# Performance work log

Measured on AMD Instinct MI355X. Metric: run time of the kernel, lower is better.

The kernel has to match this reference:

```python
import jax, jax.numpy as jnp
import numpy as np

B, S, NI, H = 64, 200, 50000, 256

def setup_inputs() -> dict:
    key = jax.random.key(0)
    ks = jax.random.split(key, 10)
    # trailing-padded sequences: lengths in [S//2, S]
    lengths = jax.random.randint(ks[0], (B,), S // 2, S + 1)
    t = jnp.arange(S)
    valid = t[None, :] < lengths[:, None]
    items = jnp.where(valid, jax.random.randint(ks[1], (B, S), 1, NI), 0)
    actions = jnp.where(valid, jax.random.randint(ks[2], (B, S), 0, 2), 0)
    sc = 1.0 / np.sqrt(H)
    # W_ih of nn.LSTM is [4H, 2*NI]; store transposed [2*NI, 4H] so one-hot matmul == row gather
    WihT = jax.random.uniform(ks[3], (2 * NI, 4 * H), jnp.float32, -sc, sc)
    Whh = jax.random.uniform(ks[4], (4 * H, H), jnp.float32, -sc, sc)
    b_lstm = jax.random.uniform(ks[5], (4 * H,), jnp.float32, -sc, sc)  # b_ih + b_hh
    trans_emb = jax.random.normal(ks[6], (NI, H), jnp.float32) * 0.05
    trans_emb = trans_emb.at[0].set(0.0)  # padding_idx=0
    Wq = jax.random.normal(ks[7], (2, H), jnp.float32) * sc
    bq = jnp.zeros((2,), jnp.float32)
    return {"items": items, "actions": actions, "WihT": WihT, "Whh": Whh,
            "b_lstm": b_lstm, "trans_emb": trans_emb, "Wq": Wq, "bq": bq}

def reference(items, actions, WihT, Whh, b_lstm, trans_emb, Wq, bq):
    ni = trans_emb.shape[0]
    h_dim = Whh.shape[1]
    it = items[:, :-1]    # [B,T]
    ac = actions[:, :-1]  # [B,T]
    mask = (it != 0)      # [B,T]
    # cat(one_hot(items,NI), one_hot(actions,NI)) @ W_ih.T == gather of two rows of WihT
    x_proj = (WihT[it] + WihT[ni + ac]) * mask[..., None].astype(WihT.dtype)  # [B,T,4H]

    def step(carry, inp):
        h, c = carry
        xp, m = inp  # xp: [B,4H], m: [B] bool
        gates = xp + h @ Whh.T + b_lstm
        i, f, g, o = jnp.split(gates, 4, axis=-1)  # torch gate order: i,f,g,o
        i = jax.nn.sigmoid(i); f = jax.nn.sigmoid(f)
        g = jnp.tanh(g);       o = jax.nn.sigmoid(o)
        c_new = f * c + i * g
        h_new = o * jnp.tanh(c_new)
        m = m[:, None]
        c = jnp.where(m, c_new, c)   # packed seq: state frozen past length
        h = jnp.where(m, h_new, h)
        out = jnp.where(m, h_new, 0.0)  # pad_packed pads outputs with zeros
        return (h, c), out

    b = items.shape[0]
    h0 = jnp.zeros((b, h_dim), WihT.dtype)
    (_, _), outs = jax.lax.scan(step, (h0, h0), (jnp.swapaxes(x_proj, 0, 1), mask.T))
    states = jnp.swapaxes(outs, 0, 1)  # [B,T,H]

    q_it = items[:, 1:]
    emb = trans_emb.at[0].set(0.0)[q_it]          # padding_idx=0 -> zero row
    query = (emb * states) @ Wq.T + bq            # [B,T,2]
    valid = (q_it != 0)
    targets = jnp.where(valid, actions[:, 1:], 0)
    logp = jax.nn.log_softmax(query, axis=-1)
    nll = -jnp.take_along_axis(logp, targets[..., None], axis=-1)[..., 0]
    vf = valid.astype(nll.dtype)
    # masked mean == F.cross_entropy over gathered (rows, cols) logits
    loss = jnp.sum(nll * vf) / jnp.sum(vf)
    return loss
```

## Files before the change

kernel.cpp:

```cpp
#include <hip/hip_runtime.h>
#include <stdint.h>

#define NITEMS 50000
#define SEQ    200
#define TMAX   199


template<int CTRL>
__device__ __forceinline__ float dpp_add(float x) {
    int r = __builtin_amdgcn_update_dpp(0, __float_as_int(x), CTRL, 0xF, 0xF, true);
    return x + __int_as_float(r);
}

__global__ __launch_bounds__(512, 2)
void lstm_main(const int* __restrict__ items, const int* __restrict__ actions,
               const float* __restrict__ WihT, const float* __restrict__ Whh,
               const float* __restrict__ b_lstm, const float* __restrict__ trans_emb,
               const float* __restrict__ Wq, const float* __restrict__ bq,
               int* flags, float* h_buf, float* accum)
{
    const int bid  = blockIdx.x;
    const int g    = (bid & 7) + 8 * ((bid >> 3) >> 2);
    const int q    = (bid >> 3) & 3;
    const int tid  = threadIdx.x;
    const int lane = tid & 63;
    const int wv   = tid >> 6;
    const int rg   = tid >> 4;
    const int kc   = tid & 15;

    __shared__ float xp_lds[2][256];
    __shared__ float gate_lds[256];
    __shared__ float b_lds[256];
    __shared__ float emb_lds[2][256];
    __shared__ float wq_lds[2][256];
    __shared__ float bq_lds[2];
    __shared__ int   items_s[SEQ];
    __shared__ int   act_s[SEQ];
    __shared__ int   len_sh;

    for (int i = tid; i < SEQ; i += 512) {
        items_s[i] = items[g * SEQ + i];
        act_s[i]   = actions[g * SEQ + i];
    }
    if (tid < 256) {
        b_lds[tid] = b_lstm[(tid >> 6) * 256 + q * 64 + (tid & 63)];
    } else {
        const int k = tid - 256;
        wq_lds[0][k] = Wq[k];
        wq_lds[1][k] = Wq[256 + k];
    }
    if (tid == 0) { bq_lds[0] = bq[0]; bq_lds[1] = bq[1]; }
    __syncthreads();
    if (tid == 0) {
        int L = 0;
        while (L < SEQ && items_s[L] != 0) ++L;
        len_sh = L;
    }
    __syncthreads();
    const int len = len_sh;
    const int L   = min(len, TMAX);

    float wgt[8][16];
    #pragma unroll
    for (int r = 0; r < 8; ++r) {
        const int r_blk = rg * 8 + r;
        const int j = (r_blk >> 6) * 256 + q * 64 + (r_blk & 63);
        const float4* wp = (const float4*)(Whh + (size_t)j * 256 + kc * 16);
        #pragma unroll
        for (int m = 0; m < 4; ++m) {
            float4 v = wp[m];
            wgt[r][4*m+0] = v.x; wgt[r][4*m+1] = v.y;
            wgt[r][4*m+2] = v.z; wgt[r][4*m+3] = v.w;
        }
    }

    if (wv == 0) {
        const int it = items_s[0], ac = act_s[0];
        const int c = lane >> 4, off = (lane & 15) * 4;
        float4 va = *(const float4*)(WihT + (size_t)it * 1024 + c * 256 + q * 64 + off);
        float4 vb = *(const float4*)(WihT + (size_t)(NITEMS + ac) * 1024 + c * 256 + q * 64 + off);
        *(float4*)&xp_lds[0][c * 64 + off] =
            make_float4(va.x+vb.x, va.y+vb.y, va.z+vb.z, va.w+vb.w);
    }
    if (q == 0 && wv == 2) {
        const int qe = items_s[1];
        float4 e = make_float4(0.f,0.f,0.f,0.f);
        if (qe != 0) e = *(const float4*)(trans_emb + (size_t)qe * 256 + 4 * lane);
        *(float4*)&emb_lds[0][4 * lane] = e;
    }
    __syncthreads();

    float c_cell = 0.f;
    float nll_acc = 0.f, cnt_acc = 0.f;
    float hreg[16];
    #pragma unroll
    for (int m = 0; m < 16; ++m) hreg[m] = 0.f;

    int*   myflags = flags + g * 32;
    float* hb      = h_buf + (size_t)g * 512;

    for (int t = 0; t < L; ++t) {
        if (t > 0) {
            if (tid < 4 && tid != q) {
                int guard = 0;
                while (__hip_atomic_load(&myflags[tid], __ATOMIC_ACQUIRE,
                                         __HIP_MEMORY_SCOPE_AGENT) < t) {
                    __builtin_amdgcn_s_sleep(1);
                    if (++guard > (1 << 16)) break;
                }
            }
            __syncthreads();
            unsigned long long* hp = (unsigned long long*)(hb + (t & 1) * 256 + kc * 16);
            #pragma unroll
            for (int m = 0; m < 8; ++m) {
                unsigned long long u = __hip_atomic_load(&hp[m], __ATOMIC_RELAXED,
                                                         __HIP_MEMORY_SCOPE_AGENT);
                union { unsigned long long u; float f[2]; } cv; cv.u = u;
                hreg[2*m]   = cv.f[0];
                hreg[2*m+1] = cv.f[1];
            }
        }

        const int tn = t + 1;
        float4 xa = make_float4(0,0,0,0), xb = make_float4(0,0,0,0);
        float4 ev = make_float4(0,0,0,0);
        float  he[4] = {0,0,0,0};
        if (wv == 1 && tn < L) {
            const int it = items_s[tn], ac = act_s[tn];
            const int c = lane >> 4, off = (lane & 15) * 4;
            xa = *(const float4*)(WihT + (size_t)it * 1024 + c * 256 + q * 64 + off);
            xb = *(const float4*)(WihT + (size_t)(NITEMS + ac) * 1024 + c * 256 + q * 64 + off);
        }
        if (q == 0 && wv == 2) {
            const int qe = items_s[tn];
            if (qe != 0) ev = *(const float4*)(trans_emb + (size_t)qe * 256 + 4 * lane);
            if (t >= 1) {
                unsigned long long* hp2 = (unsigned long long*)(hb + (t & 1) * 256 + 4 * lane);
                unsigned long long u0 = __hip_atomic_load(&hp2[0], __ATOMIC_RELAXED,
                                                          __HIP_MEMORY_SCOPE_AGENT);
                unsigned long long u1 = __hip_atomic_load(&hp2[1], __ATOMIC_RELAXED,
                                                          __HIP_MEMORY_SCOPE_AGENT);
                union { unsigned long long u; float f[2]; } c0, c1; c0.u = u0; c1.u = u1;
                he[0] = c0.f[0]; he[1] = c0.f[1]; he[2] = c1.f[0]; he[3] = c1.f[1];
            }
        }

        float acc[8];
        #pragma unroll
        for (int r = 0; r < 8; ++r) acc[r] = 0.f;
        #pragma unroll
        for (int m = 0; m < 16; ++m) {
            #pragma unroll
            for (int r = 0; r < 8; ++r) acc[r] = fmaf(wgt[r][m], hreg[m], acc[r]);
        }
        #pragma unroll
        for (int r = 0; r < 8; ++r) {
            float v = acc[r];
            v = dpp_add<0x128>(v);
            v = dpp_add<0x124>(v);
            v = dpp_add<0x122>(v);
            v = dpp_add<0x121>(v);
            acc[r] = v;
        }
        if (kc == 0) {
            #pragma unroll
            for (int r = 0; r < 8; ++r) {
                const int r_blk = rg * 8 + r;
                gate_lds[r_blk] = acc[r] + xp_lds[t & 1][r_blk] + b_lds[r_blk];
            }
        }
        __syncthreads();

        if (tid < 64) {
            const int d = tid;
            float gi = gate_lds[d];
            float gf = gate_lds[64 + d];
            float gg = gate_lds[128 + d];
            float go = gate_lds[192 + d];
            float ii = 1.f / (1.f + __expf(-gi));
            float ff = 1.f / (1.f + __expf(-gf));
            float oo = 1.f / (1.f + __expf(-go));
            float gt = tanhf(gg);
            c_cell = ff * c_cell + ii * gt;
            float hn = oo * tanhf(c_cell);
            __hip_atomic_store(&hb[((t + 1) & 1) * 256 + q * 64 + d], hn,
                               __ATOMIC_RELAXED, __HIP_MEMORY_SCOPE_AGENT);
            if (d == 0)
                __hip_atomic_store(&myflags[q], t + 1,
                                   __ATOMIC_RELEASE, __HIP_MEMORY_SCOPE_AGENT);
        } else if (wv == 1) {
            if (tn < L) {
                const int c = lane >> 4, off = (lane & 15) * 4;
                *(float4*)&xp_lds[tn & 1][c * 64 + off] =
                    make_float4(xa.x+xb.x, xa.y+xb.y, xa.z+xb.z, xa.w+xb.w);
            }
        } else if (wv == 2 && q == 0) {
            if (t >= 1) {
                const float* eb = &emb_lds[(t - 1) & 1][0];
                float s0 = 0.f, s1 = 0.f;
                #pragma unroll
                for (int m = 0; m < 4; ++m) {
                    const int k = 4 * lane + m;
                    float p = eb[k] * he[m];
                    s0 = fmaf(p, wq_lds[0][k], s0);
                    s1 = fmaf(p, wq_lds[1][k], s1);
                }
                #pragma unroll
                for (int off2 = 32; off2; off2 >>= 1) {
                    s0 += __shfl_xor(s0, off2);
                    s1 += __shfl_xor(s1, off2);
                }
                if (lane == 0) {
                    const int tgt = act_s[t];
                    float z0 = s0 + bq_lds[0], z1 = s1 + bq_lds[1];
                    float mz = fmaxf(z0, z1);
                    float lse = mz + __logf(__expf(z0 - mz) + __expf(z1 - mz));
                    nll_acc += lse - (tgt ? z1 : z0);
                    cnt_acc += 1.f;
                }
            }
            *(float4*)&emb_lds[t & 1][4 * lane] = ev;
        }
        __syncthreads();
    }

    if (q == 0 && wv == 2) {
        if (items_s[L] != 0) {
            if (lane < 4) {
                int guard = 0;
                while (__hip_atomic_load(&myflags[lane], __ATOMIC_ACQUIRE,
                                         __HIP_MEMORY_SCOPE_AGENT) < L) {
                    __builtin_amdgcn_s_sleep(1);
                    if (++guard > (1 << 16)) break;
                }
            }
            unsigned long long* hp2 = (unsigned long long*)(hb + (L & 1) * 256 + 4 * lane);
            unsigned long long u0 = __hip_atomic_load(&hp2[0], __ATOMIC_RELAXED,
                                                      __HIP_MEMORY_SCOPE_AGENT);
            unsigned long long u1 = __hip_atomic_load(&hp2[1], __ATOMIC_RELAXED,
                                                      __HIP_MEMORY_SCOPE_AGENT);
            union { unsigned long long u; float f[2]; } c0, c1; c0.u = u0; c1.u = u1;
            float he2[4] = { c0.f[0], c0.f[1], c1.f[0], c1.f[1] };
            const float* eb = &emb_lds[(L - 1) & 1][0];
            float s0 = 0.f, s1 = 0.f;
            #pragma unroll
            for (int m = 0; m < 4; ++m) {
                const int k = 4 * lane + m;
                float p = eb[k] * he2[m];
                s0 = fmaf(p, wq_lds[0][k], s0);
                s1 = fmaf(p, wq_lds[1][k], s1);
            }
            #pragma unroll
            for (int off2 = 32; off2; off2 >>= 1) {
                s0 += __shfl_xor(s0, off2);
                s1 += __shfl_xor(s1, off2);
            }
            if (lane == 0) {
                const int tgt = act_s[L];
                float z0 = s0 + bq_lds[0], z1 = s1 + bq_lds[1];
                float mz = fmaxf(z0, z1);
                float lse = mz + __logf(__expf(z0 - mz) + __expf(z1 - mz));
                nll_acc += lse - (tgt ? z1 : z0);
                cnt_acc += 1.f;
            }
        }
        if (lane == 0) {
            atomicAdd(&accum[0], nll_acc);
            atomicAdd(&accum[1], cnt_acc);
        }
    }
}

__global__ void finalize_k(const float* __restrict__ accum, float* __restrict__ out) {
    out[0] = accum[0] / accum[1];
}

extern "C" void kernel_launch(void* const* d_in, const int* in_sizes, int n_in,
                              void* d_out, int out_size, void* d_ws, size_t ws_size,
                              hipStream_t stream)
{
    const int*   items     = (const int*)d_in[0];
    const int*   actions   = (const int*)d_in[1];
    const float* WihT      = (const float*)d_in[2];
    const float* Whh       = (const float*)d_in[3];
    const float* b_lstm    = (const float*)d_in[4];
    const float* trans_emb = (const float*)d_in[5];
    const float* Wq        = (const float*)d_in[6];
    const float* bq        = (const float*)d_in[7];

    char*  ws    = (char*)d_ws;
    int*   flags = (int*)ws;
    float* accum = (float*)(ws + 8192);
    float* h_buf = (float*)(ws + 12288);

    hipMemsetAsync(d_ws, 0, 12288 + 64 * 2 * 256 * 4, stream);

    lstm_main<<<dim3(256), dim3(512), 0, stream>>>(
        items, actions, WihT, Whh, b_lstm, trans_emb, Wq, bq, flags, h_buf, accum);
    finalize_k<<<dim3(1), dim3(1), 0, stream>>>(accum, (float*)d_out);
}
```

Measured before the change: 1.499 ms.

## Batch four sequences per workgroup with packed FMA and wave-wide flag polling

New measurement: 3.568 ms. +137.9%, slower.

```diff
diff --git a/kernel.cpp b/kernel.cpp
--- a/kernel.cpp
+++ b/kernel.cpp
@@ -4,12 +4,22 @@
 #define NITEMS 50000
 #define SEQ    200
 #define TMAX   199
+#define NB     4
+
+typedef float v2f __attribute__((ext_vector_type(2)));
+typedef unsigned long long u64;
 
 
 template<int CTRL>
 __device__ __forceinline__ float dpp_add(float x) {
     int r = __builtin_amdgcn_update_dpp(0, __float_as_int(x), CTRL, 0xF, 0xF, true);
     return x + __int_as_float(r);
+}
+
+__device__ __forceinline__ void ld_h2(const u64* p, float* d) {
+    u64 a = __hip_atomic_load(p, __ATOMIC_RELAXED, __HIP_MEMORY_SCOPE_AGENT);
+    union { u64 u; float f[2]; } c; c.u = a;
+    d[0] = c.f[0]; d[1] = c.f[1];
 }
 
 __global__ __launch_bounds__(512, 2)
@@ -20,27 +30,29 @@
                int* flags, float* h_buf, float* accum)
 {
     const int bid  = blockIdx.x;
-    const int g    = (bid & 7) + 8 * ((bid >> 3) >> 2);
     const int q    = (bid >> 3) & 3;
+    const int g    = (bid & 7) + 8 * (bid >> 5);
+    const int g4   = g * 4;
     const int tid  = threadIdx.x;
     const int lane = tid & 63;
     const int wv   = tid >> 6;
     const int rg   = tid >> 4;
     const int kc   = tid & 15;
 
-    __shared__ float xp_lds[2][256];
-    __shared__ float gate_lds[256];
+    __shared__ float xp_lds[2][NB][256];
+    __shared__ float gate_lds[NB][256];
     __shared__ float b_lds[256];
-    __shared__ float emb_lds[2][256];
+    __shared__ float emb_lds[2][NB][256];
     __shared__ float wq_lds[2][256];
-    __shared__ float bq_lds[2];
-    __shared__ int   items_s[SEQ];
-    __shared__ int   act_s[SEQ];
-    __shared__ int   len_sh;
-
-    for (int i = tid; i < SEQ; i += 512) {
-        items_s[i] = items[g * SEQ + i];
-        act_s[i]   = actions[g * SEQ + i];
+    __shared__ float bq_s[2];
+    __shared__ int   items_s[NB][SEQ];
+    __shared__ int   act_s[NB][SEQ];
+    __shared__ int   L_lds[NB];
+
+    for (int i = tid; i < NB * SEQ; i += 512) {
+        const int jj = i / SEQ, pos = i - jj * SEQ;
+        items_s[jj][pos] = items[(g4 + jj) * SEQ + pos];
+        act_s[jj][pos]   = actions[(g4 + jj) * SEQ + pos];
     }
     if (tid < 256) {
         b_lds[tid] = b_lstm[(tid >> 6) * 256 + q * 64 + (tid & 63)];
@@ -49,18 +61,19 @@
         wq_lds[0][k] = Wq[k];
         wq_lds[1][k] = Wq[256 + k];
     }
-    if (tid == 0) { bq_lds[0] = bq[0]; bq_lds[1] = bq[1]; }
+    if (tid == 0) { bq_s[0] = bq[0]; bq_s[1] = bq[1]; }
     __syncthreads();
-    if (tid == 0) {
-        int L = 0;
-        while (L < SEQ && items_s[L] != 0) ++L;
-        len_sh = L;
+    if (tid < NB) {
+        int Lj = 0;
+        while (Lj < SEQ && items_s[tid][Lj] != 0) ++Lj;
+        L_lds[tid] = min(Lj, TMAX);
     }
     __syncthreads();
-    const int len = len_sh;
-    const int L   = min(len, TMAX);
-
-    float wgt[8][16];
+    int Lr[NB]; int Lmax = 0;
+    #pragma unroll
+    for (int jj = 0; jj < NB; ++jj) { Lr[jj] = L_lds[jj]; Lmax = max(Lmax, Lr[jj]); }
+
+    v2f wgt2[8][8];
     #pragma unroll
     for (int r = 0; r < 8; ++r) {
         const int r_blk = rg * 8 + r;
@@ -69,139 +82,223 @@
         #pragma unroll
         for (int m = 0; m < 4; ++m) {
             float4 v = wp[m];
-            wgt[r][4*m+0] = v.x; wgt[r][4*m+1] = v.y;
-            wgt[r][4*m+2] = v.z; wgt[r][4*m+3] = v.w;
-        }
-    }
-
-    if (wv == 0) {
-        const int it = items_s[0], ac = act_s[0];
+            wgt2[r][2*m]   = (v2f){v.x, v.y};
+            wgt2[r][2*m+1] = (v2f){v.z, v.w};
+        }
+    }
+
+    if (wv >= 1 && wv <= 4) {
+        const int jj = wv - 1;
+        const int it = items_s[jj][0], ac = act_s[jj][0];
         const int c = lane >> 4, off = (lane & 15) * 4;
         float4 va = *(const float4*)(WihT + (size_t)it * 1024 + c * 256 + q * 64 + off);
         float4 vb = *(const float4*)(WihT + (size_t)(NITEMS + ac) * 1024 + c * 256 + q * 64 + off);
-        *(float4*)&xp_lds[0][c * 64 + off] =
+        *(float4*)&xp_lds[0][jj][c * 64 + off] =
             make_float4(va.x+vb.x, va.y+vb.y, va.z+vb.z, va.w+vb.w);
     }
-    if (q == 0 && wv == 2) {
-        const int qe = items_s[1];
-        float4 e = make_float4(0.f,0.f,0.f,0.f);
-        if (qe != 0) e = *(const float4*)(trans_emb + (size_t)qe * 256 + 4 * lane);
-        *(float4*)&emb_lds[0][4 * lane] = e;
-    }
     __syncthreads();
 
-    float c_cell = 0.f;
+    float c_cell[NB];
+    #pragma unroll
+    for (int jj = 0; jj < NB; ++jj) c_cell[jj] = 0.f;
     float nll_acc = 0.f, cnt_acc = 0.f;
-    float hreg[16];
+    v2f hr2[NB][8];
     #pragma unroll
-    for (int m = 0; m < 16; ++m) hreg[m] = 0.f;
-
-    int*   myflags = flags + g * 32;
-    float* hb      = h_buf + (size_t)g * 512;
-
-    for (int t = 0; t < L; ++t) {
+    for (int jj = 0; jj < NB; ++jj)
+        #pragma unroll
+        for (int m = 0; m < 8; ++m) hr2[jj][m] = (v2f){0.f, 0.f};
+
+    for (int t = 0; t < Lmax; ++t) {
         if (t > 0) {
-            if (tid < 4 && tid != q) {
-                int guard = 0;
-                while (__hip_atomic_load(&myflags[tid], __ATOMIC_ACQUIRE,
-                                         __HIP_MEMORY_SCOPE_AGENT) < t) {
-                    __builtin_amdgcn_s_sleep(1);
-                    if (++guard > (1 << 16)) break;
-                }
-            }
-            __syncthreads();
-            unsigned long long* hp = (unsigned long long*)(hb + (t & 1) * 256 + kc * 16);
-            #pragma unroll
-            for (int m = 0; m < 8; ++m) {
-                unsigned long long u = __hip_atomic_load(&hp[m], __ATOMIC_RELAXED,
-                                                         __HIP_MEMORY_SCOPE_AGENT);
-                union { unsigned long long u; float f[2]; } cv; cv.u = u;
-                hreg[2*m]   = cv.f[0];
-                hreg[2*m+1] = cv.f[1];
+            const int jjp = (lane >> 2) & 3, pp = lane & 3;
+            const bool need = (lane < 16) && (pp != q) && (t < L_lds[jjp]);
+            const int* fp = &flags[(g4 + jjp) * 32 + pp];
+            int guard = 0;
+            for (;;) {
+                int v = need ? __hip_atomic_load(fp, __ATOMIC_RELAXED,
+                                                 __HIP_MEMORY_SCOPE_AGENT)
+                             : 0x7fffffff;
+                if (__all(v >= t)) break;
+                __builtin_amdgcn_s_sleep(1);
+                if (++guard > (1 << 17)) break;
+            }
+            __threadfence();
+
+            #pragma unroll
+            for (int jj = 0; jj < NB; ++jj) {
+                if (t < Lr[jj]) {
+                    const u64* hp = (const u64*)(h_buf + (size_t)(g4 + jj) * 512
+                                                 + (t & 1) * 256 + kc * 16);
+                    #pragma unroll
+                    for (int m = 0; m < 8; ++m) {
+                        float d2[2];
+                        ld_h2(hp + m, d2);
+                        hr2[jj][m] = (v2f){d2[0], d2[1]};
+                    }
+                }
             }
         }
 
         const int tn = t + 1;
-        float4 xa = make_float4(0,0,0,0), xb = make_float4(0,0,0,0);
-        float4 ev = make_float4(0,0,0,0);
-        float  he[4] = {0,0,0,0};
-        if (wv == 1 && tn < L) {
-            const int it = items_s[tn], ac = act_s[tn];
-            const int c = lane >> 4, off = (lane & 15) * 4;
-            xa = *(const float4*)(WihT + (size_t)it * 1024 + c * 256 + q * 64 + off);
-            xb = *(const float4*)(WihT + (size_t)(NITEMS + ac) * 1024 + c * 256 + q * 64 + off);
-        }
-        if (q == 0 && wv == 2) {
-            const int qe = items_s[tn];
-            if (qe != 0) ev = *(const float4*)(trans_emb + (size_t)qe * 256 + 4 * lane);
-            if (t >= 1) {
-                unsigned long long* hp2 = (unsigned long long*)(hb + (t & 1) * 256 + 4 * lane);
-                unsigned long long u0 = __hip_atomic_load(&hp2[0], __ATOMIC_RELAXED,
-                                                          __HIP_MEMORY_SCOPE_AGENT);
-                unsigned long long u1 = __hip_atomic_load(&hp2[1], __ATOMIC_RELAXED,
-                                                          __HIP_MEMORY_SCOPE_AGENT);
-                union { unsigned long long u; float f[2]; } c0, c1; c0.u = u0; c1.u = u1;
-                he[0] = c0.f[0]; he[1] = c0.f[1]; he[2] = c1.f[0]; he[3] = c1.f[1];
-            }
-        }
-
-        float acc[8];
+        float4 xa, xb;
+        float4 ev[NB];
+        float  her[2][4];
+        if (wv >= 1 && wv <= 4) {
+            const int jj = wv - 1;
+            if (tn < L_lds[jj]) {
+                const int it = items_s[jj][tn], ac = act_s[jj][tn];
+                const int c = lane >> 4, off = (lane & 15) * 4;
+                xa = *(const float4*)(WihT + (size_t)it * 1024 + c * 256 + q * 64 + off);
+                xb = *(const float4*)(WihT + (size_t)(NITEMS + ac) * 1024 + c * 256 + q * 64 + off);
+            }
+        } else if (wv == 5 && q == 0) {
+            #pragma unroll
+            for (int jj = 0; jj < NB; ++jj) {
+                if (t < Lr[jj]) {
+                    const int qe = items_s[jj][t + 1];
+                    ev[jj] = make_float4(0.f, 0.f, 0.f, 0.f);
+                    if (qe != 0)
+                        ev[jj] = *(const float4*)(trans_emb + (size_t)qe * 256 + 4 * lane);
+                }
+            }
+        } else if ((wv == 6 || wv == 7) && q == 0 && t > 0) {
+            #pragma unroll
+            for (int jb = 0; jb < 2; ++jb) {
+                const int jj = ((wv - 6) << 1) + jb;
+                if (t < L_lds[jj]) {
+                    const u64* hp = (const u64*)(h_buf + (size_t)(g4 + jj) * 512
+                                                 + (t & 1) * 256 + 4 * lane);
+                    ld_h2(hp,     &her[jb][0]);
+                    ld_h2(hp + 1, &her[jb][2]);
+                }
+            }
+        }
+
         #pragma unroll
-        for (int r = 0; r < 8; ++r) acc[r] = 0.f;
+        for (int jj = 0; jj < NB; ++jj) {
+            if (t < Lr[jj]) {
+                v2f acc2[8];
+                #pragma unroll
+                for (int r = 0; r < 8; ++r) acc2[r] = (v2f){0.f, 0.f};
+                #pragma unroll
+                for (int m = 0; m < 8; ++m)
+                    #pragma unroll
+                    for (int r = 0; r < 8; ++r)
+                        acc2[r] = __builtin_elementwise_fma(wgt2[r][m], hr2[jj][m], acc2[r]);
+                #pragma unroll
+                for (int r = 0; r < 8; ++r) {
+                    float v = acc2[r].x + acc2[r].y;
+                    v = dpp_add<0x128>(v);
+                    v = dpp_add<0x124>(v);
+                    v = dpp_add<0x122>(v);
+                    v = dpp_add<0x121>(v);
+                    if (kc == 0) {
+                        const int r_blk = rg * 8 + r;
+                        gate_lds[jj][r_blk] = v + xp_lds[t & 1][jj][r_blk] + b_lds[r_blk];
+                    }
+                }
+            }
+        }
+        __syncthreads();
+
+        if (tid < 64) {
+            const int d = lane;
+            #pragma unroll
+            for (int jj = 0; jj < NB; ++jj) {
+                if (t < Lr[jj]) {
+                    float gi = gate_lds[jj][d];
+                    float gf = gate_lds[jj][64 + d];
+                    float gg = gate_lds[jj][128 + d];
+                    float go = gate_lds[jj][192 + d];
+                    float ii = 1.f / (1.f + __expf(-gi));
+                    float ff = 1.f / (1.f + __expf(-gf));
+                    float oo = 1.f / (1.f + __expf(-go));
+                    float gt = tanhf(gg);
+                    c_cell[jj] = ff * c_cell[jj] + ii * gt;
+                    float hn = oo * tanhf(c_cell[jj]);
+                    __hip_atomic_store(&h_buf[(size_t)(g4 + jj) * 512
+                                              + ((t + 1) & 1) * 256 + q * 64 + d],
+                                       hn, __ATOMIC_RELAXED, __HIP_MEMORY_SCOPE_AGENT);
+                }
+            }
+            if (lane < NB) {
+                if (t < L_lds[lane])
+                    __hip_atomic_store(&flags[(g4 + lane) * 32 + q], t + 1,
+                                       __ATOMIC_RELEASE, __HIP_MEMORY_SCOPE_AGENT);
+            }
+        } else if (wv >= 1 && wv <= 4) {
+            const int jj = wv - 1;
+            if (tn < L_lds[jj]) {
+                const int c = lane >> 4, off = (lane & 15) * 4;
+                *(float4*)&xp_lds[tn & 1][jj][c * 64 + off] =
+                    make_float4(xa.x+xb.x, xa.y+xb.y, xa.z+xb.z, xa.w+xb.w);
+            }
+        } else if (wv == 5 && q == 0) {
+            #pragma unroll
+            for (int jj = 0; jj < NB; ++jj) {
+                if (t < Lr[jj])
+                    *(float4*)&emb_lds[t & 1][jj][4 * lane] = ev[jj];
+            }
+        } else if ((wv == 6 || wv == 7) && q == 0 && t > 0) {
+            #pragma unroll
+            for (int jb = 0; jb < 2; ++jb) {
+                const int jj = ((wv - 6) << 1) + jb;
+                if (t < L_lds[jj]) {
+                    const float* eb = &emb_lds[(t - 1) & 1][jj][0];
+                    float s0 = 0.f, s1 = 0.f;
+                    #pragma unroll
+                    for (int m = 0; m < 4; ++m) {
+                        const int k = 4 * lane + m;
+                        float p = eb[k] * her[jb][m];
+                        s0 = fmaf(p, wq_lds[0][k], s0);
+                        s1 = fmaf(p, wq_lds[1][k], s1);
+                    }
+                    #pragma unroll
+                    for (int off2 = 32; off2; off2 >>= 1) {
+                        s0 += __shfl_xor(s0, off2);
+                        s1 += __shfl_xor(s1, off2);
+                    }
+                    if (lane == 0) {
+                        const int tgt = act_s[jj][t];
+                        float z0 = s0 + bq_s[0], z1 = s1 + bq_s[1];
+                        float mz = fmaxf(z0, z1);
+                        float lse = mz + __logf(__expf(z0 - mz) + __expf(z1 - mz));
+                        nll_acc += lse - (tgt ? z1 : z0);
+                        cnt_acc += 1.f;
+                    }
+                }
+            }
+        }
+        __syncthreads();
+    }
+
+    if (q == 0 && (wv == 6 || wv == 7)) {
         #pragma unroll
-        for (int m = 0; m < 16; ++m) {
-            #pragma unroll
-            for (int r = 0; r < 8; ++r) acc[r] = fmaf(wgt[r][m], hreg[m], acc[r]);
-        }
-        #pragma unroll
-        for (int r = 0; r < 8; ++r) {
-            float v = acc[r];
-            v = dpp_add<0x128>(v);
-            v = dpp_add<0x124>(v);
-            v = dpp_add<0x122>(v);
-            v = dpp_add<0x121>(v);
-            acc[r] = v;
-        }
-        if (kc == 0) {
-            #pragma unroll
-            for (int r = 0; r < 8; ++r) {
-                const int r_blk = rg * 8 + r;
-                gate_lds[r_blk] = acc[r] + xp_lds[t & 1][r_blk] + b_lds[r_blk];
-            }
-        }
-        __syncthreads();
-
-        if (tid < 64) {
-            const int d = tid;
-            float gi = gate_lds[d];
-            float gf = gate_lds[64 + d];
-            float gg = gate_lds[128 + d];
-            float go = gate_lds[192 + d];
-            float ii = 1.f / (1.f + __expf(-gi));
-            float ff = 1.f / (1.f + __expf(-gf));
-            float oo = 1.f / (1.f + __expf(-go));
-            float gt = tanhf(gg);
-            c_cell = ff * c_cell + ii * gt;
-            float hn = oo * tanhf(c_cell);
-            __hip_atomic_store(&hb[((t + 1) & 1) * 256 + q * 64 + d], hn,
-                               __ATOMIC_RELAXED, __HIP_MEMORY_SCOPE_AGENT);
-            if (d == 0)
-                __hip_atomic_store(&myflags[q], t + 1,
-                                   __ATOMIC_RELEASE, __HIP_MEMORY_SCOPE_AGENT);
-        } else if (wv == 1) {
-            if (tn < L) {
-                const int c = lane >> 4, off = (lane & 15) * 4;
-                *(float4*)&xp_lds[tn & 1][c * 64 + off] =
-                    make_float4(xa.x+xb.x, xa.y+xb.y, xa.z+xb.z, xa.w+xb.w);
-            }
-        } else if (wv == 2 && q == 0) {
-            if (t >= 1) {
-                const float* eb = &emb_lds[(t - 1) & 1][0];
+        for (int jb = 0; jb < 2; ++jb) {
+            const int jj = ((wv - 6) << 1) + jb;
+            const int Lj = L_lds[jj];
+            if (items_s[jj][Lj] != 0) {
+                if (lane < 4) {
+                    int guard = 0;
+                    while (__hip_atomic_load(&flags[(g4 + jj) * 32 + lane],
+                                             __ATOMIC_RELAXED,
+                                             __HIP_MEMORY_SCOPE_AGENT) < Lj) {
+                        __builtin_amdgcn_s_sleep(1);
+                        if (++guard > (1 << 17)) break;
+                    }
+                }
+                __threadfence();
+                const u64* hp = (const u64*)(h_buf + (size_t)(g4 + jj) * 512
+                                             + (Lj & 1) * 256 + 4 * lane);
+                float he2[4];
+                ld_h2(hp,     &he2[0]);
+                ld_h2(hp + 1, &he2[2]);
+                const float* eb = &emb_lds[(Lj - 1) & 1][jj][0];
                 float s0 = 0.f, s1 = 0.f;
                 #pragma unroll
                 for (int m = 0; m < 4; ++m) {
                     const int k = 4 * lane + m;
-                    float p = eb[k] * he[m];
+                    float p = eb[k] * he2[m];
                     s0 = fmaf(p, wq_lds[0][k], s0);
                     s1 = fmaf(p, wq_lds[1][k], s1);
                 }
@@ -211,57 +308,13 @@
                     s1 += __shfl_xor(s1, off2);
                 }
                 if (lane == 0) {
-                    const int tgt = act_s[t];
-                    float z0 = s0 + bq_lds[0], z1 = s1 + bq_lds[1];
+                    const int tgt = act_s[jj][Lj];
+                    float z0 = s0 + bq_s[0], z1 = s1 + bq_s[1];
                     float mz = fmaxf(z0, z1);
                     float lse = mz + __logf(__expf(z0 - mz) + __expf(z1 - mz));
                     nll_acc += lse - (tgt ? z1 : z0);
                     cnt_acc += 1.f;
                 }
-            }
-            *(float4*)&emb_lds[t & 1][4 * lane] = ev;
-        }
-        __syncthreads();
-    }
-
-    if (q == 0 && wv == 2) {
-        if (items_s[L] != 0) {
-            if (lane < 4) {
-                int guard = 0;
-                while (__hip_atomic_load(&myflags[lane], __ATOMIC_ACQUIRE,
-                                         __HIP_MEMORY_SCOPE_AGENT) < L) {
-                    __builtin_amdgcn_s_sleep(1);
-                    if (++guard > (1 << 16)) break;
-                }
-            }
-            unsigned long long* hp2 = (unsigned long long*)(hb + (L & 1) * 256 + 4 * lane);
-            unsigned long long u0 = __hip_atomic_load(&hp2[0], __ATOMIC_RELAXED,
-                                                      __HIP_MEMORY_SCOPE_AGENT);
-            unsigned long long u1 = __hip_atomic_load(&hp2[1], __ATOMIC_RELAXED,
-                                                      __HIP_MEMORY_SCOPE_AGENT);
-            union { unsigned long long u; float f[2]; } c0, c1; c0.u = u0; c1.u = u1;
-            float he2[4] = { c0.f[0], c0.f[1], c1.f[0], c1.f[1] };
-            const float* eb = &emb_lds[(L - 1) & 1][0];
-            float s0 = 0.f, s1 = 0.f;
-            #pragma unroll
-            for (int m = 0; m < 4; ++m) {
-                const int k = 4 * lane + m;
-                float p = eb[k] * he2[m];
-                s0 = fmaf(p, wq_lds[0][k], s0);
-                s1 = fmaf(p, wq_lds[1][k], s1);
-            }
-            #pragma unroll
-            for (int off2 = 32; off2; off2 >>= 1) {
-                s0 += __shfl_xor(s0, off2);
-                s1 += __shfl_xor(s1, off2);
-            }
-            if (lane == 0) {
-                const int tgt = act_s[L];
-                float z0 = s0 + bq_lds[0], z1 = s1 + bq_lds[1];
-                float mz = fmaxf(z0, z1);
-                float lse = mz + __logf(__expf(z0 - mz) + __expf(z1 - mz));
-                nll_acc += lse - (tgt ? z1 : z0);
-                cnt_acc += 1.f;
             }
         }
         if (lane == 0) {
@@ -295,7 +348,7 @@
 
     hipMemsetAsync(d_ws, 0, 12288 + 64 * 2 * 256 * 4, stream);
 
-    lstm_main<<<dim3(256), dim3(512), 0, stream>>>(
+    lstm_main<<<dim3(64), dim3(512), 0, stream>>>(
         items, actions, WihT, Whh, b_lstm, trans_emb, Wq, bq, flags, h_buf, accum);
     finalize_k<<<dim3(1), dim3(1), 0, stream>>>(accum, (float*)d_out);
 }
```
